# Kernel tuning notes

Hardware: AMD Instinct MI355X
Metric: run time of the kernel (lower is better)

Reference implementation:

```python
import jax, jax.numpy as jnp
import numpy as np

F, H, S, B, T = 1024, 512, 512, 32, 128  # feat_size, hid_size, seq_len, batch, max_out_len


def setup_inputs() -> dict:
    key = jax.random.key(0)
    ks = jax.random.split(key, 20)
    sc = 0.05
    def p(k, shape):
        return jax.random.normal(k, shape, dtype=jnp.float32) * sc
    return {
        "feats": jax.random.normal(ks[0], (S, B, F), dtype=jnp.float32),
        # encoder forward-direction LSTM (PyTorch gate order i,f,g,o)
        "Wih_f": p(ks[1], (4 * H, F)), "Whh_f": p(ks[2], (4 * H, H)),
        "bih_f": p(ks[3], (4 * H,)), "bhh_f": p(ks[4], (4 * H,)),
        # encoder backward-direction LSTM
        "Wih_b": p(ks[5], (4 * H, F)), "Whh_b": p(ks[6], (4 * H, H)),
        "bih_b": p(ks[7], (4 * H,)), "bhh_b": p(ks[8], (4 * H,)),
        # decoder LSTMCell(F -> 2H)
        "Wih_d": p(ks[9], (8 * H, F)), "Whh_d": p(ks[10], (8 * H, 2 * H)),
        "bih_d": p(ks[11], (8 * H,)), "bhh_d": p(ks[12], (8 * H,)),
        # attention projections
        "W_enc": p(ks[13], (H, 2 * H)), "b_enc": p(ks[14], (H,)),
        "W_dec": p(ks[15], (H, 2 * H)), "b_dec": p(ks[16], (H,)),
        "W_v": p(ks[17], (1, H)), "b_v": p(ks[18], (1,)),
    }


def _cell(x, h, c, Wih, Whh, bih, bhh):
    g = x @ Wih.T + h @ Whh.T + bih + bhh
    i, f, gg, o = jnp.split(g, 4, axis=-1)
    c = jax.nn.sigmoid(f) * c + jax.nn.sigmoid(i) * jnp.tanh(gg)
    return jax.nn.sigmoid(o) * jnp.tanh(c), c


def _run_lstm(seq, Wih, Whh, bih, bhh, hid):
    b = seq.shape[1]
    init = (jnp.zeros((b, hid), seq.dtype), jnp.zeros((b, hid), seq.dtype))
    def step(carry, x):
        h, c = _cell(x, carry[0], carry[1], Wih, Whh, bih, bhh)
        return (h, c), h
    (h, c), hs = jax.lax.scan(step, init, seq)
    return hs, h, c


def reference(feats, Wih_f, Whh_f, bih_f, bhh_f, Wih_b, Whh_b, bih_b, bhh_b,
              Wih_d, Whh_d, bih_d, bhh_d, W_enc, b_enc, W_dec, b_dec, W_v, b_v):
    s, b, _ = feats.shape
    hs_f, hf, cf = _run_lstm(feats, Wih_f, Whh_f, bih_f, bhh_f, H)
    hs_b, hb, cb = _run_lstm(feats[::-1], Wih_b, Whh_b, bih_b, bhh_b, H)
    enc_out = jnp.concatenate([hs_f, hs_b[::-1]], axis=-1)  # [S,B,2H]
    # torch h.view((B, -1)) on [2,B,H] is a raw reshape, reproduced exactly
    h0 = jnp.stack([hf, hb]).reshape(b, 2 * H)
    c0 = jnp.stack([cf, cb]).reshape(b, 2 * H)
    enc_proj = enc_out @ W_enc.T + b_enc  # [S,B,H], hoisted out of the step loop
    bidx = jnp.arange(b)

    def dec_step(carry, _):
        h, c, inp = carry
        h, c = _cell(inp, h, c, Wih_d, Whh_d, bih_d, bhh_d)
        dproj = h @ W_dec.T + b_dec  # [B,H]
        scores = (jnp.tanh(enc_proj + dproj[None]) @ W_v.T + b_v)[..., 0].T  # [B,S]
        idx = jnp.argmax(scores, axis=1)  # greedy pointer (is_train=False path)
        nxt = feats[idx, bidx]  # [B,F]
        return (h, c, nxt), scores

    _, ys = jax.lax.scan(dec_step, (h0, c0, feats[0]), None, length=T)  # [T,B,S]
    return ys.reshape(T * b, s)
```

## Files before the change

kernel.cpp:

```cpp
#include <hip/hip_runtime.h>
#include <stdint.h>


#define NWG 256

__device__ __forceinline__ float sigm(float x) { return 1.0f / (1.0f + __expf(-x)); }
__device__ __forceinline__ float tanhx(float x) {
  float e = __expf(2.0f * x);
  return 1.0f - 2.0f / (e + 1.0f);
}

__device__ __forceinline__ float ldc(const float* p) {
  return __hip_atomic_load(p, __ATOMIC_RELAXED, __HIP_MEMORY_SCOPE_AGENT);
}
__device__ __forceinline__ float2 ldc2(const float* p) {
  double d = __hip_atomic_load((const double*)p, __ATOMIC_RELAXED, __HIP_MEMORY_SCOPE_AGENT);
  return __builtin_bit_cast(float2, d);
}
__device__ __forceinline__ void stc(float* p, float v) {
  __hip_atomic_store(p, v, __ATOMIC_RELAXED, __HIP_MEMORY_SCOPE_AGENT);
}
__device__ __forceinline__ int ldci(const int* p) {
  return __hip_atomic_load(p, __ATOMIC_RELAXED, __HIP_MEMORY_SCOPE_AGENT);
}
__device__ __forceinline__ void stci(int* p, int v) {
  __hip_atomic_store(p, v, __ATOMIC_RELAXED, __HIP_MEMORY_SCOPE_AGENT);
}

__device__ __forceinline__ void tree_barrier(int* bar, int w, int epoch) {
  __syncthreads();
  if (threadIdx.x == 0) {
    const int g = w >> 3;
    int* gc = bar + g * 64;
    int* rc = bar + 2048;
    int* gf = bar + 2112 + g * 64;
    int old = __hip_atomic_fetch_add(gc, 1, __ATOMIC_RELAXED, __HIP_MEMORY_SCOPE_AGENT);
    if (old == epoch * 8 - 1) {
      __hip_atomic_fetch_add(rc, 1, __ATOMIC_RELAXED, __HIP_MEMORY_SCOPE_AGENT);
      while (__hip_atomic_load(rc, __ATOMIC_RELAXED, __HIP_MEMORY_SCOPE_AGENT) < epoch * 32)
        __builtin_amdgcn_s_sleep(2);
      __hip_atomic_store(gf, epoch, __ATOMIC_RELAXED, __HIP_MEMORY_SCOPE_AGENT);
    } else {
      while (__hip_atomic_load(gf, __ATOMIC_RELAXED, __HIP_MEMORY_SCOPE_AGENT) < epoch)
        __builtin_amdgcn_s_sleep(2);
    }
  }
  __syncthreads();
}

__global__ __launch_bounds__(1024) void encoder_kernel(
    const float* __restrict__ feats,
    const float* __restrict__ Wih_f, const float* __restrict__ Whh_f,
    const float* __restrict__ bih_f, const float* __restrict__ bhh_f,
    const float* __restrict__ Wih_b, const float* __restrict__ Whh_b,
    const float* __restrict__ bih_b, const float* __restrict__ bhh_b,
    const float* __restrict__ W_enc, const float* __restrict__ b_enc,
    float* __restrict__ enc_proj, float* __restrict__ henc,
    float* __restrict__ cfin, int* __restrict__ bar)
{
  extern __shared__ __align__(16) float dyn[];
  float* wih_l = dyn;
  float* whh_l = dyn + 16448;
  __shared__ float hch[32 * 260];
  __shared__ float wenc[4 * 516];
  __shared__ float gpartK[2][32][17];
  __shared__ float projp[2][2][128];
  __shared__ float bias_s[16];
  __shared__ float benc_s[4];

  const int w = blockIdx.x;
  const int dir = (w >= 128) ? 1 : 0;
  const int wl = w & 127;
  const int col0 = wl * 4;
  const int t = threadIdx.x;
  const int kk2 = t >> 9;
  const int u = t & 511;
  const int g = u >> 7;
  const int tt = u & 127;
  const int b = tt >> 2;
  const int ci = tt & 3;
  const int col = col0 + ci;
  const int p0b = t >> 6,          p0q = t & 63;
  const int p1b = (t + 1024) >> 6, p1q = (t + 1024) & 63;

  const float* Wih = dir ? Wih_b : Wih_f;
  const float* Whh = dir ? Whh_b : Whh_f;
  const float* bih = dir ? bih_b : bih_f;
  const float* bhh = dir ? bhh_b : bhh_f;

  for (int i = t; i < 16 * 256; i += 1024) {
    int r = i >> 8, q = i & 255;
    int gg = r >> 2, cj = r & 3;
    *(float4*)(wih_l + r * 1028 + q * 4) =
        *(const float4*)(Wih + (size_t)(gg * 512 + col0 + cj) * 1024 + q * 4);
  }
  for (int i = t; i < 16 * 128; i += 1024) {
    int r = i >> 7, q = i & 127;
    int gg = r >> 2, cj = r & 3;
    *(float4*)(whh_l + r * 516 + q * 4) =
        *(const float4*)(Whh + (size_t)(gg * 512 + col0 + cj) * 512 + q * 4);
  }
  for (int i = t; i < 4 * 128; i += 1024) {
    int jl = i >> 7, q = i & 127;
    *(float4*)(wenc + jl * 516 + q * 4) =
        *(const float4*)(W_enc + (size_t)(col0 + jl) * 1024 + dir * 512 + q * 4);
  }
  if (t < 16) {
    int gg = t >> 2, cj = t & 3;
    bias_s[t] = bih[gg * 512 + col0 + cj] + bhh[gg * 512 + col0 + cj];
  }
  if (t < 4) benc_s[t] = b_enc[col0 + t];
  float c_reg = 0.0f;
  __syncthreads();

  const float* wx = wih_l + (g * 4 + ci) * 1028;
  const float* wh = whh_l + (g * 4 + ci) * 516;
  const float* wpe = wenc + ci * 516;
  const int kq = kk2 * 2 + g;

  for (int it = 0; it < 512; ++it) {
    const int s = dir ? (511 - it) : it;
    float acc = 0.0f, projacc = 0.0f;
    const float* fsrc = feats + ((size_t)s * 32) * 1024;
    const float* hsrc = henc + dir * 32768 + ((it - 1) & 1) * 16384;

    float2 h00a, h00b, h01a, h01b;
    float2 h10a, h10b, h11a, h11b;
    if (it > 0) {
      const float* sp;
      sp = hsrc + p0b * 512 + p0q * 4;       h00a = ldc2(sp); h00b = ldc2(sp + 2);
      sp = hsrc + p1b * 512 + p1q * 4;       h01a = ldc2(sp); h01b = ldc2(sp + 2);
      sp = hsrc + p0b * 512 + 256 + p0q * 4; h10a = ldc2(sp); h10b = ldc2(sp + 2);
      sp = hsrc + p1b * 512 + 256 + p1q * 4; h11a = ldc2(sp); h11b = ldc2(sp + 2);
    }

    {
      float4 xv0 = *(const float4*)(fsrc + p0b * 1024 + p0q * 4);
      float4 xv1 = *(const float4*)(fsrc + p1b * 1024 + p1q * 4);
      for (int ch = 0; ch < 4; ++ch) {
        *(float4*)(hch + p0b * 260 + p0q * 4) = xv0;
        *(float4*)(hch + p1b * 260 + p1q * 4) = xv1;
        __syncthreads();
        if (ch < 3) {
          xv0 = *(const float4*)(fsrc + p0b * 1024 + (ch + 1) * 256 + p0q * 4);
          xv1 = *(const float4*)(fsrc + p1b * 1024 + (ch + 1) * 256 + p1q * 4);
        }
        const float* hrow = hch + b * 260 + kk2 * 128;
        const float* pw = wx + ch * 256 + kk2 * 128;
#pragma unroll 8
        for (int q = 0; q < 32; ++q) {
          float4 f4 = *(const float4*)(hrow + q * 4);
          float4 a4 = *(const float4*)(pw + q * 4);
          acc += f4.x * a4.x + f4.y * a4.y + f4.z * a4.z + f4.w * a4.w;
        }
        __syncthreads();
      }
    }

    if (it > 0) {
      *(float4*)(hch + p0b * 260 + p0q * 4) = make_float4(h00a.x, h00a.y, h00b.x, h00b.y);
      *(float4*)(hch + p1b * 260 + p1q * 4) = make_float4(h01a.x, h01a.y, h01b.x, h01b.y);
      __syncthreads();
      {
        const float* hrow = hch + b * 260 + kk2 * 128;
        const float* pw = wh + kk2 * 128;
#pragma unroll 8
        for (int q = 0; q < 32; ++q) {
          float4 h4 = *(const float4*)(hrow + q * 4);
          float4 a4 = *(const float4*)(pw + q * 4);
          acc += h4.x * a4.x + h4.y * a4.y + h4.z * a4.z + h4.w * a4.w;
        }
        if (g < 2) {
          const float* hp = hch + b * 260 + kq * 64;
          const float* wp = wpe + kq * 64;
#pragma unroll 4
          for (int kk = 0; kk < 16; ++kk) {
            float4 h4 = *(const float4*)(hp + kk * 4);
            float4 w4 = *(const float4*)(wp + kk * 4);
            projacc += h4.x * w4.x + h4.y * w4.y + h4.z * w4.z + h4.w * w4.w;
          }
        }
      }
      __syncthreads();
      *(float4*)(hch + p0b * 260 + p0q * 4) = make_float4(h10a.x, h10a.y, h10b.x, h10b.y);
      *(float4*)(hch + p1b * 260 + p1q * 4) = make_float4(h11a.x, h11a.y, h11b.x, h11b.y);
      __syncthreads();
      {
        const float* hrow = hch + b * 260 + kk2 * 128;
        const float* pw = wh + 256 + kk2 * 128;
#pragma unroll 8
        for (int q = 0; q < 32; ++q) {
          float4 h4 = *(const float4*)(hrow + q * 4);
          float4 a4 = *(const float4*)(pw + q * 4);
          acc += h4.x * a4.x + h4.y * a4.y + h4.z * a4.z + h4.w * a4.w;
        }
        if (g < 2) {
          const float* hp = hch + b * 260 + kq * 64;
          const float* wp = wpe + 256 + kq * 64;
#pragma unroll 4
          for (int kk = 0; kk < 16; ++kk) {
            float4 h4 = *(const float4*)(hp + kk * 4);
            float4 w4 = *(const float4*)(wp + kk * 4);
            projacc += h4.x * w4.x + h4.y * w4.y + h4.z * w4.z + h4.w * w4.w;
          }
        }
      }
      __syncthreads();
    }

    gpartK[kk2][b][g * 4 + ci] = acc;
    if (g < 2) projp[kk2][g][tt] = projacc;
    __syncthreads();
    if (t < 128) {
      float gi = gpartK[0][b][ci + 0] + gpartK[1][b][ci + 0] + bias_s[ci + 0];
      float gf = gpartK[0][b][ci + 4] + gpartK[1][b][ci + 4] + bias_s[ci + 4];
      float gg = gpartK[0][b][ci + 8] + gpartK[1][b][ci + 8] + bias_s[ci + 8];
      float go = gpartK[0][b][ci + 12] + gpartK[1][b][ci + 12] + bias_s[ci + 12];
      float cn = sigm(gf) * c_reg + sigm(gi) * tanhx(gg);
      c_reg = cn;
      stc(henc + dir * 32768 + (it & 1) * 16384 + b * 512 + col,
          sigm(go) * tanhx(cn));
    } else if (kk2 == 0 && g == 1 && it > 0) {
      const int sp = dir ? (512 - it) : (it - 1);
      const float p = projp[0][0][tt] + projp[0][1][tt] +
                      projp[1][0][tt] + projp[1][1][tt];
      float* addr = enc_proj + ((size_t)sp * 32 + b) * 512 + col;
      if (it - 1 <= 255) {
        stc(addr, p + benc_s[ci]);
      } else {
        stc(addr, ldc(addr) + p);
      }
    }
    tree_barrier(bar, w, it + 1);
  }

  {
    const float* hsrc = henc + dir * 32768 + 16384;
    float projacc = 0.0f;
    for (int ch = 0; ch < 2; ++ch) {
      for (int i = t; i < 2048; i += 1024) {
        int bb = i >> 6, qf = i & 63;
        const float* sp = hsrc + bb * 512 + ch * 256 + qf * 4;
        float2 f0 = ldc2(sp);
        float2 f1 = ldc2(sp + 2);
        *(float4*)(hch + bb * 260 + qf * 4) = make_float4(f0.x, f0.y, f1.x, f1.y);
      }
      __syncthreads();
      if (g < 2) {
        const float* hp = hch + b * 260 + kq * 64;
        const float* wp = wpe + ch * 256 + kq * 64;
#pragma unroll 4
        for (int kk = 0; kk < 16; ++kk) {
          float4 h4 = *(const float4*)(hp + kk * 4);
          float4 w4 = *(const float4*)(wp + kk * 4);
          projacc += h4.x * w4.x + h4.y * w4.y + h4.z * w4.z + h4.w * w4.w;
        }
      }
      __syncthreads();
    }
    if (g < 2) projp[kk2][g][tt] = projacc;
    __syncthreads();
    if (kk2 == 0 && g == 1) {
      const int sp = dir ? 0 : 511;
      float* addr = enc_proj + ((size_t)sp * 32 + b) * 512 + col;
      stc(addr, ldc(addr) + (projp[0][0][tt] + projp[0][1][tt] +
                             projp[1][0][tt] + projp[1][1][tt]));
    }
    if (t < 128) cfin[dir * 16384 + b * 512 + col] = c_reg;
  }
}

__global__ __launch_bounds__(512) void decoder_kernel(
    const float* __restrict__ feats,
    const float* __restrict__ Wih_d, const float* __restrict__ Whh_d,
    const float* __restrict__ bih_d, const float* __restrict__ bhh_d,
    const float* __restrict__ W_dec, const float* __restrict__ b_dec,
    const float* __restrict__ W_v, const float* __restrict__ b_v,
    const float* __restrict__ enc_proj, const float* __restrict__ henc,
    const float* __restrict__ cfin,
    float* __restrict__ hbuf, float* __restrict__ dproj,
    float* __restrict__ pval, int* __restrict__ pidx,
    int* __restrict__ bar, float* __restrict__ out)
{
  extern __shared__ __align__(16) float dyn[];
  float* whh_l = dyn;
  float* wih_l = dyn + 16448;
  __shared__ float hch[32 * 132];
  __shared__ float gpart[2][32][17];
  __shared__ float c_lds[32][4];
  __shared__ float bias_s[16];
  __shared__ float svals[64];
  __shared__ int ib_lds[32];
  float* dpl = hch + 1088;

  const int w = blockIdx.x;
  const int t = threadIdx.x;
  const int q4 = t >> 7;
  const int tt = t & 127;
  const int b = tt >> 2;
  const int ci = tt & 3;
  const int col0 = w * 4;
  const int col = col0 + ci;
  const int i0 = t, i1 = t + 512;
  const int bb0 = i0 >> 5, q0 = i0 & 31;
  const int bb1 = i1 >> 5, q1 = i1 & 31;
  const int bb_c = w >> 3;
  const int qq_ = w & 7;
  const int ccB = t >> 8;
  const int bB = (t >> 3) & 31;
  const int k8 = t & 7;

  for (int i = t; i < 16 * 256; i += 512) {
    int r = i >> 8, q = i & 255;
    int gg = r >> 2, cj = r & 3;
    *(float4*)(whh_l + r * 1028 + q * 4) =
        *(const float4*)(Whh_d + (size_t)(gg * 1024 + col0 + cj) * 1024 + q * 4);
    *(float4*)(wih_l + r * 1028 + q * 4) =
        *(const float4*)(Wih_d + (size_t)(gg * 1024 + col0 + cj) * 1024 + q * 4);
  }
  if (t < 16) {
    int gg = t >> 2, cj = t & 3;
    bias_s[t] = bih_d[gg * 1024 + col0 + cj] + bhh_d[gg * 1024 + col0 + cj];
  }
  if (t < 128) {
    int flat = b * 1024 + col;
    int d = flat >> 14, sb = (flat >> 9) & 31, sh = flat & 511;
    float h0, c0;
    if (d == 0) {
      h0 = henc[16384 + sb * 512 + sh];
      c0 = cfin[sb * 512 + sh];
    } else {
      h0 = henc[32768 + 16384 + sb * 512 + sh];
      c0 = cfin[16384 + sb * 512 + sh];
    }
    stc(hbuf + b * 1024 + col, h0);
    c_lds[b][ci] = c0;
  }
  int bars = 1;
  tree_barrier(bar, w, bars);

  const float* wbase = (q4 < 2) ? whh_l : wih_l;
  const int g0 = (q4 & 1) * 2;
  const float* wr0 = wbase + (size_t)((g0 + 0) * 4 + ci) * 1028;
  const float* wr1 = wbase + (size_t)((g0 + 1) * 4 + ci) * 1028;

  for (int ts = 0; ts < 128; ++ts) {
    const float* hprev = hbuf + (ts & 1) * 32768;
    float* hnext = hbuf + ((ts + 1) & 1) * 32768;

    float a0 = 0.f, a1 = 0.f;
    const float* xrow = nullptr;
    {
      float2 s0a0 = ldc2(hprev + bb0 * 1024 + q0 * 4);
      float2 s0a1 = ldc2(hprev + bb0 * 1024 + q0 * 4 + 2);
      float2 s0b0 = ldc2(hprev + bb1 * 1024 + q1 * 4);
      float2 s0b1 = ldc2(hprev + bb1 * 1024 + q1 * 4 + 2);
      float2 s1a0 = ldc2(hprev + bb0 * 1024 + 128 + q0 * 4);
      float2 s1a1 = ldc2(hprev + bb0 * 1024 + 128 + q0 * 4 + 2);
      float2 s1b0 = ldc2(hprev + bb1 * 1024 + 128 + q1 * 4);
      float2 s1b1 = ldc2(hprev + bb1 * 1024 + 128 + q1 * 4 + 2);
      if (t < 32) {
        int ib = 0;
        if (ts > 0) {
          float v = ldc(pval + t * 8 + 0);
          int si = ldci(pidx + t * 8 + 0);
#pragma unroll
          for (int j = 1; j < 8; ++j) {
            float ov = ldc(pval + t * 8 + j);
            int os = ldci(pidx + t * 8 + j);
            if (ov > v || (ov == v && os < si)) { v = ov; si = os; }
          }
          ib = si;
        }
        ib_lds[t] = ib;
      }
      for (int ch = 0; ch < 8; ++ch) {
        if (ch & 1) {
          *(float4*)(hch + bb0 * 132 + q0 * 4) = make_float4(s1a0.x, s1a0.y, s1a1.x, s1a1.y);
          *(float4*)(hch + bb1 * 132 + q1 * 4) = make_float4(s1b0.x, s1b0.y, s1b1.x, s1b1.y);
        } else {
          *(float4*)(hch + bb0 * 132 + q0 * 4) = make_float4(s0a0.x, s0a0.y, s0a1.x, s0a1.y);
          *(float4*)(hch + bb1 * 132 + q1 * 4) = make_float4(s0b0.x, s0b0.y, s0b1.x, s0b1.y);
        }
        __syncthreads();
        if (ch == 0 && q4 >= 2) {
          int ib = ib_lds[b];
          xrow = feats + ((size_t)ib * 32 + b) * 1024;
        }
        if (ch < 6) {
          const int cn = (ch + 2) * 128;
          if (ch & 1) {
            s1a0 = ldc2(hprev + bb0 * 1024 + cn + q0 * 4);
            s1a1 = ldc2(hprev + bb0 * 1024 + cn + q0 * 4 + 2);
            s1b0 = ldc2(hprev + bb1 * 1024 + cn + q1 * 4);
            s1b1 = ldc2(hprev + bb1 * 1024 + cn + q1 * 4 + 2);
          } else {
            s0a0 = ldc2(hprev + bb0 * 1024 + cn + q0 * 4);
            s0a1 = ldc2(hprev + bb0 * 1024 + cn + q0 * 4 + 2);
            s0b0 = ldc2(hprev + bb1 * 1024 + cn + q1 * 4);
            s0b1 = ldc2(hprev + bb1 * 1024 + cn + q1 * 4 + 2);
          }
        }
        const float* src = (q4 < 2) ? (hch + b * 132) : (xrow + ch * 128);
        const float* p0 = wr0 + ch * 128;
        const float* p1 = wr1 + ch * 128;
#pragma unroll 8
        for (int qq = 0; qq < 32; ++qq) {
          float4 h4 = *(const float4*)(src + qq * 4);
          float4 u0 = *(const float4*)(p0 + qq * 4);
          float4 u1 = *(const float4*)(p1 + qq * 4);
          a0 += h4.x * u0.x + h4.y * u0.y + h4.z * u0.z + h4.w * u0.w;
          a1 += h4.x * u1.x + h4.y * u1.y + h4.z * u1.z + h4.w * u1.w;
        }
        __syncthreads();
      }
    }
    gpart[q4 >> 1][b][ci + (g0 + 0) * 4] = a0;
    gpart[q4 >> 1][b][ci + (g0 + 1) * 4] = a1;
    __syncthreads();
    if (t < 128) {
      float gi = gpart[0][b][ci + 0] + gpart[1][b][ci + 0] + bias_s[ci + 0];
      float gf = gpart[0][b][ci + 4] + gpart[1][b][ci + 4] + bias_s[ci + 4];
      float gg = gpart[0][b][ci + 8] + gpart[1][b][ci + 8] + bias_s[ci + 8];
      float go = gpart[0][b][ci + 12] + gpart[1][b][ci + 12] + bias_s[ci + 12];
      float cn = sigm(gf) * c_lds[b][ci] + sigm(gi) * tanhx(gg);
      c_lds[b][ci] = cn;
      stc(hnext + b * 1024 + col, sigm(go) * tanhx(cn));
    }
    ++bars; tree_barrier(bar, w, bars);

    {
      float dacc = 0.f;
      const float* wdrow = W_dec + (size_t)(2 * w + ccB) * 1024;
      float2 s0a0 = ldc2(hnext + bb0 * 1024 + q0 * 4);
      float2 s0a1 = ldc2(hnext + bb0 * 1024 + q0 * 4 + 2);
      float2 s0b0 = ldc2(hnext + bb1 * 1024 + q1 * 4);
      float2 s0b1 = ldc2(hnext + bb1 * 1024 + q1 * 4 + 2);
      float2 s1a0 = ldc2(hnext + bb0 * 1024 + 128 + q0 * 4);
      float2 s1a1 = ldc2(hnext + bb0 * 1024 + 128 + q0 * 4 + 2);
      float2 s1b0 = ldc2(hnext + bb1 * 1024 + 128 + q1 * 4);
      float2 s1b1 = ldc2(hnext + bb1 * 1024 + 128 + q1 * 4 + 2);
      for (int ch = 0; ch < 8; ++ch) {
        if (ch & 1) {
          *(float4*)(hch + bb0 * 132 + q0 * 4) = make_float4(s1a0.x, s1a0.y, s1a1.x, s1a1.y);
          *(float4*)(hch + bb1 * 132 + q1 * 4) = make_float4(s1b0.x, s1b0.y, s1b1.x, s1b1.y);
        } else {
          *(float4*)(hch + bb0 * 132 + q0 * 4) = make_float4(s0a0.x, s0a0.y, s0a1.x, s0a1.y);
          *(float4*)(hch + bb1 * 132 + q1 * 4) = make_float4(s0b0.x, s0b0.y, s0b1.x, s0b1.y);
        }
        __syncthreads();
        if (ch < 6) {
          const int cn = (ch + 2) * 128;
          if (ch & 1) {
            s1a0 = ldc2(hnext + bb0 * 1024 + cn + q0 * 4);
            s1a1 = ldc2(hnext + bb0 * 1024 + cn + q0 * 4 + 2);
            s1b0 = ldc2(hnext + bb1 * 1024 + cn + q1 * 4);
            s1b1 = ldc2(hnext + bb1 * 1024 + cn + q1 * 4 + 2);
          } else {
            s0a0 = ldc2(hnext + bb0 * 1024 + cn + q0 * 4);
            s0a1 = ldc2(hnext + bb0 * 1024 + cn + q0 * 4 + 2);
            s0b0 = ldc2(hnext + bb1 * 1024 + cn + q1 * 4);
            s0b1 = ldc2(hnext + bb1 * 1024 + cn + q1 * 4 + 2);
          }
        }
        const float* hl = hch + bB * 132 + k8 * 16;
        const float* wl = wdrow + ch * 128 + k8 * 16;
#pragma unroll
        for (int j = 0; j < 4; ++j) {
          float4 h4 = *(const float4*)(hl + j * 4);
          float4 w4 = *(const float4*)(wl + j * 4);
          dacc += h4.x * w4.x + h4.y * w4.y + h4.z * w4.z + h4.w * w4.w;
        }
        __syncthreads();
      }
      dacc += __shfl_xor(dacc, 1);
      dacc += __shfl_xor(dacc, 2);
      dacc += __shfl_xor(dacc, 4);
      if (k8 == 0) stc(dproj + bB * 512 + 2 * w + ccB, dacc + b_dec[2 * w + ccB]);
    }
    ++bars; tree_barrier(bar, w, bars);

    if (t < 256) {
      float2 v = ldc2(dproj + bb_c * 512 + 2 * t);
      int k = 2 * t;
      dpl[(k >> 6) * 68 + (k & 63) + 0] = v.x;
      dpl[(k >> 6) * 68 + (k & 63) + 1] = v.y;
    }
    __syncthreads();
    {
      const int sl = t >> 3, ks = t & 7;
      const int s = qq_ * 64 + sl;
      const float* ep = enc_proj + ((size_t)s * 32 + bb_c) * 512 + ks * 64;
      const float* dpp = dpl + ks * 68;
      const float* wvp = W_v + ks * 64;
      float sum = 0.f;
#pragma unroll 4
      for (int j = 0; j < 16; ++j) {
        float4 e4 = *(const float4*)(ep + j * 4);
        float4 d4 = *(const float4*)(dpp + j * 4);
        float4 v4 = *(const float4*)(wvp + j * 4);
        sum += tanhx(e4.x + d4.x) * v4.x;
        sum += tanhx(e4.y + d4.y) * v4.y;
        sum += tanhx(e4.z + d4.z) * v4.z;
        sum += tanhx(e4.w + d4.w) * v4.w;
      }
      sum += __shfl_xor(sum, 1);
      sum += __shfl_xor(sum, 2);
      sum += __shfl_xor(sum, 4);
      if (ks == 0) {
        float sv = sum + b_v[0];
        out[((size_t)ts * 32 + bb_c) * 512 + s] = sv;
        svals[sl] = sv;
      }
    }
    __syncthreads();
    if (t < 64) {
      float v = svals[t];
      int si = qq_ * 64 + t;
#pragma unroll
      for (int m = 1; m < 64; m <<= 1) {
        float ov = __shfl_xor(v, m);
        int os = __shfl_xor(si, m);
        if (ov > v || (ov == v && os < si)) { v = ov; si = os; }
      }
      if (t == 0) {
        stc(pval + bb_c * 8 + qq_, v);
        stci(pidx + bb_c * 8 + qq_, si);
      }
    }
    ++bars; tree_barrier(bar, w, bars);
  }
}

extern "C" void kernel_launch(void* const* d_in, const int* in_sizes, int n_in,
                              void* d_out, int out_size, void* d_ws, size_t ws_size,
                              hipStream_t stream) {
  (void)in_sizes; (void)n_in; (void)out_size; (void)ws_size;
  const float* feats = (const float*)d_in[0];
  const float* Wih_f = (const float*)d_in[1];
  const float* Whh_f = (const float*)d_in[2];
  const float* bih_f = (const float*)d_in[3];
  const float* bhh_f = (const float*)d_in[4];
  const float* Wih_b = (const float*)d_in[5];
  const float* Whh_b = (const float*)d_in[6];
  const float* bih_b = (const float*)d_in[7];
  const float* bhh_b = (const float*)d_in[8];
  const float* Wih_d = (const float*)d_in[9];
  const float* Whh_d = (const float*)d_in[10];
  const float* bih_d = (const float*)d_in[11];
  const float* bhh_d = (const float*)d_in[12];
  const float* W_enc = (const float*)d_in[13];
  const float* b_enc = (const float*)d_in[14];
  const float* W_dec = (const float*)d_in[15];
  const float* b_dec = (const float*)d_in[16];
  const float* W_v   = (const float*)d_in[17];
  const float* b_v   = (const float*)d_in[18];
  float* out = (float*)d_out;

  int* ctrl = (int*)d_ws;
  int* bar_enc = ctrl;
  int* bar_dec = ctrl + 8192;
  float* base = (float*)d_ws + 16384;
  float* enc_proj = base;
  float* henc     = enc_proj + 8388608;
  float* cfin     = henc + 65536;
  float* hbuf     = cfin + 32768;
  float* dproj    = hbuf + 65536;
  float* pval     = dproj + 16384;
  int*   pidx     = (int*)(pval + 8192);

  const int ENC_LDS = (16 * 1028 + 16 * 516) * 4;
  const int DEC_LDS = (2 * 16 * 1028) * 4;
  hipFuncSetAttribute((const void*)encoder_kernel,
                      hipFuncAttributeMaxDynamicSharedMemorySize, ENC_LDS);
  hipFuncSetAttribute((const void*)decoder_kernel,
                      hipFuncAttributeMaxDynamicSharedMemorySize, DEC_LDS);

  hipMemsetAsync(d_ws, 0, 65536, stream);

  {
    void* args[] = {(void*)&feats,
                    (void*)&Wih_f, (void*)&Whh_f, (void*)&bih_f, (void*)&bhh_f,
                    (void*)&Wih_b, (void*)&Whh_b, (void*)&bih_b, (void*)&bhh_b,
                    (void*)&W_enc, (void*)&b_enc,
                    (void*)&enc_proj, (void*)&henc, (void*)&cfin, (void*)&bar_enc};
    hipLaunchCooperativeKernel((const void*)encoder_kernel, dim3(NWG), dim3(1024),
                               args, ENC_LDS, stream);
  }
  {
    void* args[] = {(void*)&feats,
                    (void*)&Wih_d, (void*)&Whh_d, (void*)&bih_d, (void*)&bhh_d,
                    (void*)&W_dec, (void*)&b_dec, (void*)&W_v, (void*)&b_v,
                    (void*)&enc_proj, (void*)&henc, (void*)&cfin,
                    (void*)&hbuf, (void*)&dproj, (void*)&pval, (void*)&pidx,
                    (void*)&bar_dec, (void*)&out};
    hipLaunchCooperativeKernel((const void*)decoder_kernel, dim3(NWG), dim3(512),
                               args, DEC_LDS, stream);
  }
}
```

Baseline: 16.75 ms.

## Double decoder threads with K-split reductions and prefetch next encoder input

The decoder now launches 1024 threads per workgroup instead of 512. The gate matvec, the W_dec projection and the attention score dot products are each split along K across twice as many threads, with partial sums reduced via an extra LDS partial dimension or an extra shuffle stage. Separately, the encoder loads the next timestep's feats slice before the grid barrier, so that global load overlaps the barrier wait. The intent is to shorten the per-step latency of the serial recurrences, at the cost of more register pressure under launch_bounds(1024) and more reduction work.

```diff
diff --git a/kernel.cpp b/kernel.cpp
--- a/kernel.cpp
+++ b/kernel.cpp
@@ -118,6 +118,10 @@
   const float* wpe = wenc + ci * 516;
   const int kq = kk2 * 2 + g;
 
+  const int s0_ = dir ? 511 : 0;
+  float4 fx0 = *(const float4*)(feats + ((size_t)s0_ * 32) * 1024 + p0b * 1024 + p0q * 4);
+  float4 fx1 = *(const float4*)(feats + ((size_t)s0_ * 32) * 1024 + p1b * 1024 + p1q * 4);
+
   for (int it = 0; it < 512; ++it) {
     const int s = dir ? (511 - it) : it;
     float acc = 0.0f, projacc = 0.0f;
@@ -135,8 +139,8 @@
     }
 
     {
-      float4 xv0 = *(const float4*)(fsrc + p0b * 1024 + p0q * 4);
-      float4 xv1 = *(const float4*)(fsrc + p1b * 1024 + p1q * 4);
+      float4 xv0 = fx0;
+      float4 xv1 = fx1;
       for (int ch = 0; ch < 4; ++ch) {
         *(float4*)(hch + p0b * 260 + p0q * 4) = xv0;
         *(float4*)(hch + p1b * 260 + p1q * 4) = xv1;
@@ -231,6 +235,12 @@
         stc(addr, ldc(addr) + p);
       }
     }
+    {
+      const int sn = (it < 511) ? (dir ? (510 - it) : (it + 1)) : s;
+      const float* fn = feats + ((size_t)sn * 32) * 1024;
+      fx0 = *(const float4*)(fn + p0b * 1024 + p0q * 4);
+      fx1 = *(const float4*)(fn + p1b * 1024 + p1q * 4);
+    }
     tree_barrier(bar, w, it + 1);
   }
 
@@ -270,7 +280,7 @@
   }
 }
 
-__global__ __launch_bounds__(512) void decoder_kernel(
+__global__ __launch_bounds__(1024) void decoder_kernel(
     const float* __restrict__ feats,
     const float* __restrict__ Wih_d, const float* __restrict__ Whh_d,
     const float* __restrict__ bih_d, const float* __restrict__ bhh_d,
@@ -286,7 +296,7 @@
   float* whh_l = dyn;
   float* wih_l = dyn + 16448;
   __shared__ float hch[32 * 132];
-  __shared__ float gpart[2][32][17];
+  __shared__ float gpartK[2][2][32][17];
   __shared__ float c_lds[32][4];
   __shared__ float bias_s[16];
   __shared__ float svals[64];
@@ -295,22 +305,22 @@
 
   const int w = blockIdx.x;
   const int t = threadIdx.x;
-  const int q4 = t >> 7;
-  const int tt = t & 127;
+  const int kk2A = t >> 9;
+  const int u = t & 511;
+  const int q4 = u >> 7;
+  const int tt = u & 127;
   const int b = tt >> 2;
   const int ci = tt & 3;
   const int col0 = w * 4;
   const int col = col0 + ci;
-  const int i0 = t, i1 = t + 512;
-  const int bb0 = i0 >> 5, q0 = i0 & 31;
-  const int bb1 = i1 >> 5, q1 = i1 & 31;
+  const int bbS = t >> 5, qqS = t & 31;
   const int bb_c = w >> 3;
   const int qq_ = w & 7;
-  const int ccB = t >> 8;
-  const int bB = (t >> 3) & 31;
-  const int k8 = t & 7;
-
-  for (int i = t; i < 16 * 256; i += 512) {
+  const int ccB = t >> 9;
+  const int bB = (t >> 4) & 31;
+  const int k16 = t & 15;
+
+  for (int i = t; i < 16 * 256; i += 1024) {
     int r = i >> 8, q = i & 255;
     int gg = r >> 2, cj = r & 3;
     *(float4*)(whh_l + r * 1028 + q * 4) =
@@ -341,8 +351,8 @@
 
   const float* wbase = (q4 < 2) ? whh_l : wih_l;
   const int g0 = (q4 & 1) * 2;
-  const float* wr0 = wbase + (size_t)((g0 + 0) * 4 + ci) * 1028;
-  const float* wr1 = wbase + (size_t)((g0 + 1) * 4 + ci) * 1028;
+  const float* wr0 = wbase + (size_t)((g0 + 0) * 4 + ci) * 1028 + kk2A * 64;
+  const float* wr1 = wbase + (size_t)((g0 + 1) * 4 + ci) * 1028 + kk2A * 64;
 
   for (int ts = 0; ts < 128; ++ts) {
     const float* hprev = hbuf + (ts & 1) * 32768;
@@ -351,14 +361,10 @@
     float a0 = 0.f, a1 = 0.f;
     const float* xrow = nullptr;
     {
-      float2 s0a0 = ldc2(hprev + bb0 * 1024 + q0 * 4);
-      float2 s0a1 = ldc2(hprev + bb0 * 1024 + q0 * 4 + 2);
-      float2 s0b0 = ldc2(hprev + bb1 * 1024 + q1 * 4);
-      float2 s0b1 = ldc2(hprev + bb1 * 1024 + q1 * 4 + 2);
-      float2 s1a0 = ldc2(hprev + bb0 * 1024 + 128 + q0 * 4);
-      float2 s1a1 = ldc2(hprev + bb0 * 1024 + 128 + q0 * 4 + 2);
-      float2 s1b0 = ldc2(hprev + bb1 * 1024 + 128 + q1 * 4);
-      float2 s1b1 = ldc2(hprev + bb1 * 1024 + 128 + q1 * 4 + 2);
+      float2 pA0 = ldc2(hprev + bbS * 1024 + qqS * 4);
+      float2 pA1 = ldc2(hprev + bbS * 1024 + qqS * 4 + 2);
+      float2 pB0 = ldc2(hprev + bbS * 1024 + 128 + qqS * 4);
+      float2 pB1 = ldc2(hprev + bbS * 1024 + 128 + qqS * 4 + 2);
       if (t < 32) {
         int ib = 0;
         if (ts > 0) {
@@ -376,11 +382,9 @@
       }
       for (int ch = 0; ch < 8; ++ch) {
         if (ch & 1) {
-          *(float4*)(hch + bb0 * 132 + q0 * 4) = make_float4(s1a0.x, s1a0.y, s1a1.x, s1a1.y);
-          *(float4*)(hch + bb1 * 132 + q1 * 4) = make_float4(s1b0.x, s1b0.y, s1b1.x, s1b1.y);
+          *(float4*)(hch + bbS * 132 + qqS * 4) = make_float4(pB0.x, pB0.y, pB1.x, pB1.y);
         } else {
-          *(float4*)(hch + bb0 * 132 + q0 * 4) = make_float4(s0a0.x, s0a0.y, s0a1.x, s0a1.y);
-          *(float4*)(hch + bb1 * 132 + q1 * 4) = make_float4(s0b0.x, s0b0.y, s0b1.x, s0b1.y);
+          *(float4*)(hch + bbS * 132 + qqS * 4) = make_float4(pA0.x, pA0.y, pA1.x, pA1.y);
         }
         __syncthreads();
         if (ch == 0 && q4 >= 2) {
@@ -390,22 +394,19 @@
         if (ch < 6) {
           const int cn = (ch + 2) * 128;
           if (ch & 1) {
-            s1a0 = ldc2(hprev + bb0 * 1024 + cn + q0 * 4);
-            s1a1 = ldc2(hprev + bb0 * 1024 + cn + q0 * 4 + 2);
-            s1b0 = ldc2(hprev + bb1 * 1024 + cn + q1 * 4);
-            s1b1 = ldc2(hprev + bb1 * 1024 + cn + q1 * 4 + 2);
+            pB0 = ldc2(hprev + bbS * 1024 + cn + qqS * 4);
+            pB1 = ldc2(hprev + bbS * 1024 + cn + qqS * 4 + 2);
           } else {
-            s0a0 = ldc2(hprev + bb0 * 1024 + cn + q0 * 4);
-            s0a1 = ldc2(hprev + bb0 * 1024 + cn + q0 * 4 + 2);
-            s0b0 = ldc2(hprev + bb1 * 1024 + cn + q1 * 4);
-            s0b1 = ldc2(hprev + bb1 * 1024 + cn + q1 * 4 + 2);
+            pA0 = ldc2(hprev + bbS * 1024 + cn + qqS * 4);
+            pA1 = ldc2(hprev + bbS * 1024 + cn + qqS * 4 + 2);
           }
         }
-        const float* src = (q4 < 2) ? (hch + b * 132) : (xrow + ch * 128);
+        const float* src = (q4 < 2) ? (hch + b * 132 + kk2A * 64)
+                                    : (xrow + ch * 128 + kk2A * 64);
         const float* p0 = wr0 + ch * 128;
         const float* p1 = wr1 + ch * 128;
-#pragma unroll 8
-        for (int qq = 0; qq < 32; ++qq) {
+#pragma unroll
+        for (int qq = 0; qq < 16; ++qq) {
           float4 h4 = *(const float4*)(src + qq * 4);
           float4 u0 = *(const float4*)(p0 + qq * 4);
           float4 u1 = *(const float4*)(p1 + qq * 4);
@@ -415,14 +416,18 @@
         __syncthreads();
       }
     }
-    gpart[q4 >> 1][b][ci + (g0 + 0) * 4] = a0;
-    gpart[q4 >> 1][b][ci + (g0 + 1) * 4] = a1;
+    gpartK[kk2A][q4 >> 1][b][ci + (g0 + 0) * 4] = a0;
+    gpartK[kk2A][q4 >> 1][b][ci + (g0 + 1) * 4] = a1;
     __syncthreads();
     if (t < 128) {
-      float gi = gpart[0][b][ci + 0] + gpart[1][b][ci + 0] + bias_s[ci + 0];
-      float gf = gpart[0][b][ci + 4] + gpart[1][b][ci + 4] + bias_s[ci + 4];
-      float gg = gpart[0][b][ci + 8] + gpart[1][b][ci + 8] + bias_s[ci + 8];
-      float go = gpart[0][b][ci + 12] + gpart[1][b][ci + 12] + bias_s[ci + 12];
+      float gi = (gpartK[0][0][b][ci + 0] + gpartK[0][1][b][ci + 0]) +
+                 (gpartK[1][0][b][ci + 0] + gpartK[1][1][b][ci + 0]) + bias_s[ci + 0];
+      float gf = (gpartK[0][0][b][ci + 4] + gpartK[0][1][b][ci + 4]) +
+                 (gpartK[1][0][b][ci + 4] + gpartK[1][1][b][ci + 4]) + bias_s[ci + 4];
+      float gg = (gpartK[0][0][b][ci + 8] + gpartK[0][1][b][ci + 8]) +
+                 (gpartK[1][0][b][ci + 8] + gpartK[1][1][b][ci + 8]) + bias_s[ci + 8];
+      float go = (gpartK[0][0][b][ci + 12] + gpartK[0][1][b][ci + 12]) +
+                 (gpartK[1][0][b][ci + 12] + gpartK[1][1][b][ci + 12]) + bias_s[ci + 12];
       float cn = sigm(gf) * c_lds[b][ci] + sigm(gi) * tanhx(gg);
       c_lds[b][ci] = cn;
       stc(hnext + b * 1024 + col, sigm(go) * tanhx(cn));
@@ -432,41 +437,31 @@
     {
       float dacc = 0.f;
       const float* wdrow = W_dec + (size_t)(2 * w + ccB) * 1024;
-      float2 s0a0 = ldc2(hnext + bb0 * 1024 + q0 * 4);
-      float2 s0a1 = ldc2(hnext + bb0 * 1024 + q0 * 4 + 2);
-      float2 s0b0 = ldc2(hnext + bb1 * 1024 + q1 * 4);
-      float2 s0b1 = ldc2(hnext + bb1 * 1024 + q1 * 4 + 2);
-      float2 s1a0 = ldc2(hnext + bb0 * 1024 + 128 + q0 * 4);
-      float2 s1a1 = ldc2(hnext + bb0 * 1024 + 128 + q0 * 4 + 2);
-      float2 s1b0 = ldc2(hnext + bb1 * 1024 + 128 + q1 * 4);
-      float2 s1b1 = ldc2(hnext + bb1 * 1024 + 128 + q1 * 4 + 2);
+      float2 pA0 = ldc2(hnext + bbS * 1024 + qqS * 4);
+      float2 pA1 = ldc2(hnext + bbS * 1024 + qqS * 4 + 2);
+      float2 pB0 = ldc2(hnext + bbS * 1024 + 128 + qqS * 4);
+      float2 pB1 = ldc2(hnext + bbS * 1024 + 128 + qqS * 4 + 2);
       for (int ch = 0; ch < 8; ++ch) {
         if (ch & 1) {
-          *(float4*)(hch + bb0 * 132 + q0 * 4) = make_float4(s1a0.x, s1a0.y, s1a1.x, s1a1.y);
-          *(float4*)(hch + bb1 * 132 + q1 * 4) = make_float4(s1b0.x, s1b0.y, s1b1.x, s1b1.y);
+          *(float4*)(hch + bbS * 132 + qqS * 4) = make_float4(pB0.x, pB0.y, pB1.x, pB1.y);
         } else {
-          *(float4*)(hch + bb0 * 132 + q0 * 4) = make_float4(s0a0.x, s0a0.y, s0a1.x, s0a1.y);
-          *(float4*)(hch + bb1 * 132 + q1 * 4) = make_float4(s0b0.x, s0b0.y, s0b1.x, s0b1.y);
+          *(float4*)(hch + bbS * 132 + qqS * 4) = make_float4(pA0.x, pA0.y, pA1.x, pA1.y);
         }
         __syncthreads();
         if (ch < 6) {
           const int cn = (ch + 2) * 128;
           if (ch & 1) {
-            s1a0 = ldc2(hnext + bb0 * 1024 + cn + q0 * 4);
-            s1a1 = ldc2(hnext + bb0 * 1024 + cn + q0 * 4 + 2);
-            s1b0 = ldc2(hnext + bb1 * 1024 + cn + q1 * 4);
-            s1b1 = ldc2(hnext + bb1 * 1024 + cn + q1 * 4 + 2);
+            pB0 = ldc2(hnext + bbS * 1024 + cn + qqS * 4);
+            pB1 = ldc2(hnext + bbS * 1024 + cn + qqS * 4 + 2);
           } else {
-            s0a0 = ldc2(hnext + bb0 * 1024 + cn + q0 * 4);
-            s0a1 = ldc2(hnext + bb0 * 1024 + cn + q0 * 4 + 2);
-            s0b0 = ldc2(hnext + bb1 * 1024 + cn + q1 * 4);
-            s0b1 = ldc2(hnext + bb1 * 1024 + cn + q1 * 4 + 2);
+            pA0 = ldc2(hnext + bbS * 1024 + cn + qqS * 4);
+            pA1 = ldc2(hnext + bbS * 1024 + cn + qqS * 4 + 2);
           }
         }
-        const float* hl = hch + bB * 132 + k8 * 16;
-        const float* wl = wdrow + ch * 128 + k8 * 16;
+        const float* hl = hch + bB * 132 + k16 * 8;
+        const float* wl = wdrow + ch * 128 + k16 * 8;
 #pragma unroll
-        for (int j = 0; j < 4; ++j) {
+        for (int j = 0; j < 2; ++j) {
           float4 h4 = *(const float4*)(hl + j * 4);
           float4 w4 = *(const float4*)(wl + j * 4);
           dacc += h4.x * w4.x + h4.y * w4.y + h4.z * w4.z + h4.w * w4.w;
@@ -476,7 +471,8 @@
       dacc += __shfl_xor(dacc, 1);
       dacc += __shfl_xor(dacc, 2);
       dacc += __shfl_xor(dacc, 4);
-      if (k8 == 0) stc(dproj + bB * 512 + 2 * w + ccB, dacc + b_dec[2 * w + ccB]);
+      dacc += __shfl_xor(dacc, 8);
+      if (k16 == 0) stc(dproj + bB * 512 + 2 * w + ccB, dacc + b_dec[2 * w + ccB]);
     }
     ++bars; tree_barrier(bar, w, bars);
 
@@ -488,14 +484,14 @@
     }
     __syncthreads();
     {
-      const int sl = t >> 3, ks = t & 7;
+      const int sl = t >> 4, ks = t & 15;
       const int s = qq_ * 64 + sl;
-      const float* ep = enc_proj + ((size_t)s * 32 + bb_c) * 512 + ks * 64;
-      const float* dpp = dpl + ks * 68;
-      const float* wvp = W_v + ks * 64;
+      const float* ep = enc_proj + ((size_t)s * 32 + bb_c) * 512 + ks * 32;
+      const float* dpp = dpl + (ks >> 1) * 68 + (ks & 1) * 32;
+      const float* wvp = W_v + ks * 32;
       float sum = 0.f;
-#pragma unroll 4
-      for (int j = 0; j < 16; ++j) {
+#pragma unroll
+      for (int j = 0; j < 8; ++j) {
         float4 e4 = *(const float4*)(ep + j * 4);
         float4 d4 = *(const float4*)(dpp + j * 4);
         float4 v4 = *(const float4*)(wvp + j * 4);
@@ -507,6 +503,7 @@
       sum += __shfl_xor(sum, 1);
       sum += __shfl_xor(sum, 2);
       sum += __shfl_xor(sum, 4);
+      sum += __shfl_xor(sum, 8);
       if (ks == 0) {
         float sv = sum + b_v[0];
         out[((size_t)ts * 32 + bb_c) * 512 + s] = sv;
@@ -594,7 +591,7 @@
                     (void*)&enc_proj, (void*)&henc, (void*)&cfin,
                     (void*)&hbuf, (void*)&dproj, (void*)&pval, (void*)&pidx,
                     (void*)&bar_dec, (void*)&out};
-    hipLaunchCooperativeKernel((const void*)decoder_kernel, dim3(NWG), dim3(512),
+    hipLaunchCooperativeKernel((const void*)decoder_kernel, dim3(NWG), dim3(1024),
                                args, DEC_LDS, stream);
   }
 }
```

Measured after the change: 17.48 ms. 1.04x slower.

## Register-block encoder matvec over two batch rows and prefetch next step's features

Applied to the files above, without the earlier changes.

Remaps encoder threads so each computes two batch rows (b and b+16) over a quarter of K, so each weight float4 loaded from LDS is reused twice. The K split grows from 2 to 4 partial sums. The projection work moves onto the g==0 threads and is fused into the hidden-state loop, reusing the same h loads. The first feature chunk for the next timestep is prefetched into registers before the grid barrier, hiding global load latency behind synchronisation. The cost is more registers per thread and a larger cross-thread reduction.

```diff
diff --git a/kernel.cpp b/kernel.cpp
--- a/kernel.cpp
+++ b/kernel.cpp
@@ -63,8 +63,8 @@
   float* whh_l = dyn + 16448;
   __shared__ float hch[32 * 260];
   __shared__ float wenc[4 * 516];
-  __shared__ float gpartK[2][32][17];
-  __shared__ float projp[2][2][128];
+  __shared__ float gpartK[4][32][17];
+  __shared__ float projp[4][128];
   __shared__ float bias_s[16];
   __shared__ float benc_s[4];
 
@@ -73,13 +73,12 @@
   const int wl = w & 127;
   const int col0 = wl * 4;
   const int t = threadIdx.x;
-  const int kk2 = t >> 9;
-  const int u = t & 511;
-  const int g = u >> 7;
-  const int tt = u & 127;
-  const int b = tt >> 2;
-  const int ci = tt & 3;
-  const int col = col0 + ci;
+  const int kk4 = t >> 8;
+  const int u = t & 255;
+  const int g = u >> 6;
+  const int v = u & 63;
+  const int bp = v >> 2;
+  const int ci = v & 3;
   const int p0b = t >> 6,          p0q = t & 63;
   const int p1b = (t + 1024) >> 6, p1q = (t + 1024) & 63;
 
@@ -116,11 +115,15 @@
   const float* wx = wih_l + (g * 4 + ci) * 1028;
   const float* wh = whh_l + (g * 4 + ci) * 516;
   const float* wpe = wenc + ci * 516;
-  const int kq = kk2 * 2 + g;
+
+  const int s0_ = dir ? 511 : 0;
+  float4 fx0 = *(const float4*)(feats + ((size_t)s0_ * 32) * 1024 + p0b * 1024 + p0q * 4);
+  float4 fx1 = *(const float4*)(feats + ((size_t)s0_ * 32) * 1024 + p1b * 1024 + p1q * 4);
 
   for (int it = 0; it < 512; ++it) {
     const int s = dir ? (511 - it) : it;
-    float acc = 0.0f, projacc = 0.0f;
+    float acc0 = 0.0f, acc1 = 0.0f;
+    float pacc0 = 0.0f, pacc1 = 0.0f;
     const float* fsrc = feats + ((size_t)s * 32) * 1024;
     const float* hsrc = henc + dir * 32768 + ((it - 1) & 1) * 16384;
 
@@ -135,8 +138,8 @@
     }
 
     {
-      float4 xv0 = *(const float4*)(fsrc + p0b * 1024 + p0q * 4);
-      float4 xv1 = *(const float4*)(fsrc + p1b * 1024 + p1q * 4);
+      float4 xv0 = fx0;
+      float4 xv1 = fx1;
       for (int ch = 0; ch < 4; ++ch) {
         *(float4*)(hch + p0b * 260 + p0q * 4) = xv0;
         *(float4*)(hch + p1b * 260 + p1q * 4) = xv1;
@@ -145,98 +148,106 @@
           xv0 = *(const float4*)(fsrc + p0b * 1024 + (ch + 1) * 256 + p0q * 4);
           xv1 = *(const float4*)(fsrc + p1b * 1024 + (ch + 1) * 256 + p1q * 4);
         }
-        const float* hrow = hch + b * 260 + kk2 * 128;
-        const float* pw = wx + ch * 256 + kk2 * 128;
+        const float* aw = wx + ch * 256 + kk4 * 64;
+        const float* h0 = hch + bp * 260 + kk4 * 64;
+        const float* h1 = hch + (bp + 16) * 260 + kk4 * 64;
 #pragma unroll 8
-        for (int q = 0; q < 32; ++q) {
-          float4 f4 = *(const float4*)(hrow + q * 4);
-          float4 a4 = *(const float4*)(pw + q * 4);
-          acc += f4.x * a4.x + f4.y * a4.y + f4.z * a4.z + f4.w * a4.w;
+        for (int j = 0; j < 16; ++j) {
+          float4 w4 = *(const float4*)(aw + j * 4);
+          float4 a0 = *(const float4*)(h0 + j * 4);
+          float4 a1 = *(const float4*)(h1 + j * 4);
+          acc0 += w4.x * a0.x + w4.y * a0.y + w4.z * a0.z + w4.w * a0.w;
+          acc1 += w4.x * a1.x + w4.y * a1.y + w4.z * a1.z + w4.w * a1.w;
         }
         __syncthreads();
       }
     }
 
     if (it > 0) {
-      *(float4*)(hch + p0b * 260 + p0q * 4) = make_float4(h00a.x, h00a.y, h00b.x, h00b.y);
-      *(float4*)(hch + p1b * 260 + p1q * 4) = make_float4(h01a.x, h01a.y, h01b.x, h01b.y);
-      __syncthreads();
-      {
-        const float* hrow = hch + b * 260 + kk2 * 128;
-        const float* pw = wh + kk2 * 128;
+#pragma unroll
+      for (int ch = 0; ch < 2; ++ch) {
+        if (ch == 0) {
+          *(float4*)(hch + p0b * 260 + p0q * 4) = make_float4(h00a.x, h00a.y, h00b.x, h00b.y);
+          *(float4*)(hch + p1b * 260 + p1q * 4) = make_float4(h01a.x, h01a.y, h01b.x, h01b.y);
+        } else {
+          *(float4*)(hch + p0b * 260 + p0q * 4) = make_float4(h10a.x, h10a.y, h10b.x, h10b.y);
+          *(float4*)(hch + p1b * 260 + p1q * 4) = make_float4(h11a.x, h11a.y, h11b.x, h11b.y);
+        }
+        __syncthreads();
+        const float* aw = wh + ch * 256 + kk4 * 64;
+        const float* h0 = hch + bp * 260 + kk4 * 64;
+        const float* h1 = hch + (bp + 16) * 260 + kk4 * 64;
+        if (g == 0) {
+          const float* wp = wpe + ch * 256 + kk4 * 64;
+#pragma unroll 4
+          for (int j = 0; j < 16; ++j) {
+            float4 w4 = *(const float4*)(aw + j * 4);
+            float4 a0 = *(const float4*)(h0 + j * 4);
+            float4 a1 = *(const float4*)(h1 + j * 4);
+            float4 wp4 = *(const float4*)(wp + j * 4);
+            acc0 += w4.x * a0.x + w4.y * a0.y + w4.z * a0.z + w4.w * a0.w;
+            acc1 += w4.x * a1.x + w4.y * a1.y + w4.z * a1.z + w4.w * a1.w;
+            pacc0 += wp4.x * a0.x + wp4.y * a0.y + wp4.z * a0.z + wp4.w * a0.w;
+            pacc1 += wp4.x * a1.x + wp4.y * a1.y + wp4.z * a1.z + wp4.w * a1.w;
+          }
+        } else {
 #pragma unroll 8
-        for (int q = 0; q < 32; ++q) {
-          float4 h4 = *(const float4*)(hrow + q * 4);
-          float4 a4 = *(const float4*)(pw + q * 4);
-          acc += h4.x * a4.x + h4.y * a4.y + h4.z * a4.z + h4.w * a4.w;
-        }
-        if (g < 2) {
-          const float* hp = hch + b * 260 + kq * 64;
-          const float* wp = wpe + kq * 64;
-#pragma unroll 4
-          for (int kk = 0; kk < 16; ++kk) {
-            float4 h4 = *(const float4*)(hp + kk * 4);
-            float4 w4 = *(const float4*)(wp + kk * 4);
-            projacc += h4.x * w4.x + h4.y * w4.y + h4.z * w4.z + h4.w * w4.w;
+          for (int j = 0; j < 16; ++j) {
+            float4 w4 = *(const float4*)(aw + j * 4);
+            float4 a0 = *(const float4*)(h0 + j * 4);
+            float4 a1 = *(const float4*)(h1 + j * 4);
+            acc0 += w4.x * a0.x + w4.y * a0.y + w4.z * a0.z + w4.w * a0.w;
+            acc1 += w4.x * a1.x + w4.y * a1.y + w4.z * a1.z + w4.w * a1.w;
           }
         }
-      }
-      __syncthreads();
-      *(float4*)(hch + p0b * 260 + p0q * 4) = make_float4(h10a.x, h10a.y, h10b.x, h10b.y);
-      *(float4*)(hch + p1b * 260 + p1q * 4) = make_float4(h11a.x, h11a.y, h11b.x, h11b.y);
-      __syncthreads();
-      {
-        const float* hrow = hch + b * 260 + kk2 * 128;
-        const float* pw = wh + 256 + kk2 * 128;
-#pragma unroll 8
-        for (int q = 0; q < 32; ++q) {
-          float4 h4 = *(const float4*)(hrow + q * 4);
-          float4 a4 = *(const float4*)(pw + q * 4);
-          acc += h4.x * a4.x + h4.y * a4.y + h4.z * a4.z + h4.w * a4.w;
-        }
-        if (g < 2) {
-          const float* hp = hch + b * 260 + kq * 64;
-          const float* wp = wpe + 256 + kq * 64;
-#pragma unroll 4
-          for (int kk = 0; kk < 16; ++kk) {
-            float4 h4 = *(const float4*)(hp + kk * 4);
-            float4 w4 = *(const float4*)(wp + kk * 4);
-            projacc += h4.x * w4.x + h4.y * w4.y + h4.z * w4.z + h4.w * w4.w;
-          }
-        }
-      }
-      __syncthreads();
-    }
-
-    gpartK[kk2][b][g * 4 + ci] = acc;
-    if (g < 2) projp[kk2][g][tt] = projacc;
+        __syncthreads();
+      }
+    }
+
+    gpartK[kk4][bp][g * 4 + ci] = acc0;
+    gpartK[kk4][bp + 16][g * 4 + ci] = acc1;
+    if (g == 0) {
+      projp[kk4][bp * 4 + ci] = pacc0;
+      projp[kk4][(bp + 16) * 4 + ci] = pacc1;
+    }
     __syncthreads();
     if (t < 128) {
-      float gi = gpartK[0][b][ci + 0] + gpartK[1][b][ci + 0] + bias_s[ci + 0];
-      float gf = gpartK[0][b][ci + 4] + gpartK[1][b][ci + 4] + bias_s[ci + 4];
-      float gg = gpartK[0][b][ci + 8] + gpartK[1][b][ci + 8] + bias_s[ci + 8];
-      float go = gpartK[0][b][ci + 12] + gpartK[1][b][ci + 12] + bias_s[ci + 12];
+      const int b_ = t >> 2, ci_ = t & 3;
+      float gi = gpartK[0][b_][ci_ + 0] + gpartK[1][b_][ci_ + 0] +
+                 gpartK[2][b_][ci_ + 0] + gpartK[3][b_][ci_ + 0] + bias_s[ci_ + 0];
+      float gf = gpartK[0][b_][ci_ + 4] + gpartK[1][b_][ci_ + 4] +
+                 gpartK[2][b_][ci_ + 4] + gpartK[3][b_][ci_ + 4] + bias_s[ci_ + 4];
+      float gg = gpartK[0][b_][ci_ + 8] + gpartK[1][b_][ci_ + 8] +
+                 gpartK[2][b_][ci_ + 8] + gpartK[3][b_][ci_ + 8] + bias_s[ci_ + 8];
+      float go = gpartK[0][b_][ci_ + 12] + gpartK[1][b_][ci_ + 12] +
+                 gpartK[2][b_][ci_ + 12] + gpartK[3][b_][ci_ + 12] + bias_s[ci_ + 12];
       float cn = sigm(gf) * c_reg + sigm(gi) * tanhx(gg);
       c_reg = cn;
-      stc(henc + dir * 32768 + (it & 1) * 16384 + b * 512 + col,
+      stc(henc + dir * 32768 + (it & 1) * 16384 + b_ * 512 + col0 + ci_,
           sigm(go) * tanhx(cn));
-    } else if (kk2 == 0 && g == 1 && it > 0) {
+    } else if (t >= 128 && t < 256 && it > 0) {
+      const int l = t - 128, b_ = l >> 2, ci_ = l & 3;
       const int sp = dir ? (512 - it) : (it - 1);
-      const float p = projp[0][0][tt] + projp[0][1][tt] +
-                      projp[1][0][tt] + projp[1][1][tt];
-      float* addr = enc_proj + ((size_t)sp * 32 + b) * 512 + col;
+      const float p = projp[0][l] + projp[1][l] + projp[2][l] + projp[3][l];
+      float* addr = enc_proj + ((size_t)sp * 32 + b_) * 512 + col0 + ci_;
       if (it - 1 <= 255) {
-        stc(addr, p + benc_s[ci]);
+        stc(addr, p + benc_s[ci_]);
       } else {
         stc(addr, ldc(addr) + p);
       }
     }
+    {
+      const int sn = (it < 511) ? (dir ? (510 - it) : (it + 1)) : s;
+      const float* fn = feats + ((size_t)sn * 32) * 1024;
+      fx0 = *(const float4*)(fn + p0b * 1024 + p0q * 4);
+      fx1 = *(const float4*)(fn + p1b * 1024 + p1q * 4);
+    }
     tree_barrier(bar, w, it + 1);
   }
 
   {
     const float* hsrc = henc + dir * 32768 + 16384;
-    float projacc = 0.0f;
+    float pacc0 = 0.0f, pacc1 = 0.0f;
     for (int ch = 0; ch < 2; ++ch) {
       for (int i = t; i < 2048; i += 1024) {
         int bb = i >> 6, qf = i & 63;
@@ -246,27 +257,33 @@
         *(float4*)(hch + bb * 260 + qf * 4) = make_float4(f0.x, f0.y, f1.x, f1.y);
       }
       __syncthreads();
-      if (g < 2) {
-        const float* hp = hch + b * 260 + kq * 64;
-        const float* wp = wpe + ch * 256 + kq * 64;
+      if (g == 0) {
+        const float* wp = wpe + ch * 256 + kk4 * 64;
+        const float* h0 = hch + bp * 260 + kk4 * 64;
+        const float* h1 = hch + (bp + 16) * 260 + kk4 * 64;
 #pragma unroll 4
-        for (int kk = 0; kk < 16; ++kk) {
-          float4 h4 = *(const float4*)(hp + kk * 4);
-          float4 w4 = *(const float4*)(wp + kk * 4);
-          projacc += h4.x * w4.x + h4.y * w4.y + h4.z * w4.z + h4.w * w4.w;
+        for (int j = 0; j < 16; ++j) {
+          float4 wp4 = *(const float4*)(wp + j * 4);
+          float4 a0 = *(const float4*)(h0 + j * 4);
+          float4 a1 = *(const float4*)(h1 + j * 4);
+          pacc0 += wp4.x * a0.x + wp4.y * a0.y + wp4.z * a0.z + wp4.w * a0.w;
+          pacc1 += wp4.x * a1.x + wp4.y * a1.y + wp4.z * a1.z + wp4.w * a1.w;
         }
       }
       __syncthreads();
     }
-    if (g < 2) projp[kk2][g][tt] = projacc;
+    if (g == 0) {
+      projp[kk4][bp * 4 + ci] = pacc0;
+      projp[kk4][(bp + 16) * 4 + ci] = pacc1;
+    }
     __syncthreads();
-    if (kk2 == 0 && g == 1) {
+    if (t >= 128 && t < 256) {
+      const int l = t - 128, b_ = l >> 2, ci_ = l & 3;
       const int sp = dir ? 0 : 511;
-      float* addr = enc_proj + ((size_t)sp * 32 + b) * 512 + col;
-      stc(addr, ldc(addr) + (projp[0][0][tt] + projp[0][1][tt] +
-                             projp[1][0][tt] + projp[1][1][tt]));
-    }
-    if (t < 128) cfin[dir * 16384 + b * 512 + col] = c_reg;
+      float* addr = enc_proj + ((size_t)sp * 32 + b_) * 512 + col0 + ci_;
+      stc(addr, ldc(addr) + (projp[0][l] + projp[1][l] + projp[2][l] + projp[3][l]));
+    }
+    if (t < 128) cfin[dir * 16384 + (t >> 2) * 512 + col0 + (t & 3)] = c_reg;
   }
 }
 
```

Measured after the change: 16.25 ms. 3.0% less time.
